# Performance work log

Measured on AMD Instinct MI355X. Metric: run time of the kernel, lower is better.

Reference implementation:

```python
import jax, jax.numpy as jnp
import numpy as np

B, S, D, H, FF = 4, 2048, 1024, 16, 4096
HD = D // H


def setup_inputs() -> dict:
    key = jax.random.key(0)
    ks = jax.random.split(key, 12)
    s = 1.0 / np.sqrt(D)
    sf = 1.0 / np.sqrt(FF)
    return {
        "x": jax.random.normal(ks[0], (B, S, D), dtype=jnp.float32),
        "lengths": jax.random.randint(ks[1], (B,), 1, S + 1, dtype=jnp.int32),
        "qW": jax.random.uniform(ks[2], (D, D), jnp.float32, -s, s),
        "qb": jnp.zeros((D,), jnp.float32),
        "kW": jax.random.uniform(ks[3], (D, D), jnp.float32, -s, s),
        "kb": jnp.zeros((D,), jnp.float32),
        "vW": jax.random.uniform(ks[4], (D, D), jnp.float32, -s, s),
        "vb": jnp.zeros((D,), jnp.float32),
        "oW": jax.random.uniform(ks[5], (D, D), jnp.float32, -s, s),
        "ob": jnp.zeros((D,), jnp.float32),
        "w1": jax.random.uniform(ks[6], (D, FF), jnp.float32, -s, s),
        "b1": jnp.zeros((FF,), jnp.float32),
        "w2": jax.random.uniform(ks[7], (FF, D), jnp.float32, -sf, sf),
        "b2": jnp.zeros((D,), jnp.float32),
    }


def _heads(t):
    # [B,S,D] -> [B,H,S,HD]
    return t.reshape(B, S, H, HD).transpose(0, 2, 1, 3)


def reference(x, lengths, qW, qb, kW, kb, vW, vb, oW, ob, w1, b1, w2, b2):
    q = _heads(x @ qW + qb)
    k = _heads(x @ kW + kb)
    v = _heads(x @ vW + vb)
    scale = 1.0 / np.sqrt(HD)
    logits = jnp.einsum("bhqd,bhkd->bhqk", q, k) * scale  # [B,H,S,S]
    # key-position mask: pos >= length -> -inf
    mask = jnp.arange(S)[None, None, None, :] >= lengths[:, None, None, None]
    logits = jnp.where(mask, -jnp.inf, logits)
    a = jax.nn.softmax(logits, axis=-1)
    ctx = jnp.einsum("bhqk,bhkd->bhqd", a, v)
    ctx = ctx.transpose(0, 2, 1, 3).reshape(B, S, D)
    attn_out = ctx @ oW + ob
    h = jax.nn.relu(attn_out @ w1 + b1)
    return h @ w2 + b2
```

## Files before the change

kernel.cpp:

```cpp
#include <hip/hip_runtime.h>


typedef short bf16x8 __attribute__((ext_vector_type(8)));
typedef float f32x4 __attribute__((ext_vector_type(4)));

__device__ __forceinline__ unsigned short f2bf(float f) {
  unsigned int u = __builtin_bit_cast(unsigned int, f);
  u += 0x7fffu + ((u >> 16) & 1u);
  return (unsigned short)(u >> 16);
}

__device__ __forceinline__ void gload16(const unsigned short* g, unsigned short* l) {
  __builtin_amdgcn_global_load_lds(
      (const __attribute__((address_space(1))) unsigned int*)(g),
      (__attribute__((address_space(3))) unsigned int*)(l),
      16, 0, 0);
}

__global__ __launch_bounds__(256) void cast_f32_bf16(
    const float* __restrict__ src, unsigned short* __restrict__ dst, int n4) {
  int i = blockIdx.x * 256 + threadIdx.x;
  if (i < n4) {
    float4 f = ((const float4*)src)[i];
    ushort4 o;
    o.x = f2bf(f.x); o.y = f2bf(f.y); o.z = f2bf(f.z); o.w = f2bf(f.w);
    ((ushort4*)dst)[i] = o;
  }
}

__global__ __launch_bounds__(256) void prep_weights(
    const float* __restrict__ qW, const float* __restrict__ kW,
    const float* __restrict__ vW, const float* __restrict__ oW,
    const float* __restrict__ w1, const float* __restrict__ w2,
    unsigned short* __restrict__ qWt, unsigned short* __restrict__ kWt,
    unsigned short* __restrict__ vWt, unsigned short* __restrict__ oWt,
    unsigned short* __restrict__ w1t, unsigned short* __restrict__ w2t) {
  const int t = blockIdx.x;
  const float* W; unsigned short* Wt; int N, K, nt, kt;
  if (t < 2048) {
    const int w = t >> 9, r = t & 511;
    nt = r & 15; kt = r >> 4; N = 1024; K = 1024;
    W  = w == 0 ? qW : w == 1 ? kW : w == 2 ? vW : oW;
    Wt = w == 0 ? qWt : w == 1 ? kWt : w == 2 ? vWt : oWt;
  } else if (t < 4096) {
    const int r = t - 2048;
    nt = r & 63; kt = r >> 6; N = 4096; K = 1024; W = w1; Wt = w1t;
  } else {
    const int r = t - 4096;
    nt = r & 15; kt = r >> 4; N = 1024; K = 4096; W = w2; Wt = w2t;
  }
  const int wave = threadIdx.x >> 6, lane = threadIdx.x & 63;
  const int n = nt * 64 + lane;
  const int k0 = kt * 32 + wave * 8;
  union { int4 v; unsigned short u[8]; } s;
#pragma unroll
  for (int j = 0; j < 8; ++j) s.u[j] = f2bf(W[(size_t)(k0 + j) * N + n]);
  *(int4*)(Wt + (size_t)n * K + k0) = s.v;
}

__device__ __forceinline__ void gemm256_8ph(
    const unsigned short* __restrict__ A, const unsigned short* __restrict__ Bt,
    unsigned short* __restrict__ As, unsigned short* __restrict__ Bs,
    const int m0, const int n0, const int K, f32x4 (&acc)[8][4]) {
  const int tid = (int)threadIdx.x;
  const int w = tid >> 6, l = tid & 63;
  const int quad = l >> 4, l16 = l & 15;
  const int wm = (w >> 2) * 128, wn = (w & 3) * 64;

  const int srow = w * 8 + (l >> 3);
  const int schunk = ((l & 7) ^ (l >> 3)) * 8;
  const unsigned short* gA = A + (size_t)(m0 + srow) * K + schunk;
  const unsigned short* gB = Bt + (size_t)(n0 + srow) * K + schunk;
  const int ldsW = w * 512;

  const int xr = l16 & 7;
  const int c0 = ((0 + quad) ^ xr) * 8;
  const int c1 = ((4 + quad) ^ xr) * 8;

  bf16x8 af[4][2], bf0[2][2], bf1[2][2];

  auto STA = [&](int buf, int a, int t) {
    gload16(gA + (size_t)(a * 64) * K + t * 64,
            As + buf * 16384 + a * 4096 + ldsW);
  };
  auto STB = [&](int buf, int a, int t) {
    gload16(gB + (size_t)(a * 64) * K + t * 64,
            Bs + buf * 16384 + a * 4096 + ldsW);
  };
  auto LDA = [&](int buf, int mh) {
    const unsigned short* p = As + buf * 16384 + (wm + mh * 64 + l16) * 64;
#pragma unroll
    for (int mi = 0; mi < 4; ++mi) {
      af[mi][0] = *(const bf16x8*)(p + mi * 16 * 64 + c0);
      af[mi][1] = *(const bf16x8*)(p + mi * 16 * 64 + c1);
    }
  };
  auto LDB = [&](int buf, int nh, bf16x8 (&bf)[2][2]) {
    const unsigned short* p = Bs + buf * 16384 + (wn + nh * 32 + l16) * 64;
#pragma unroll
    for (int ni = 0; ni < 2; ++ni) {
      bf[ni][0] = *(const bf16x8*)(p + ni * 16 * 64 + c0);
      bf[ni][1] = *(const bf16x8*)(p + ni * 16 * 64 + c1);
    }
  };
  auto MM = [&](int mh, int nh, bf16x8 (&bf)[2][2]) {
    __builtin_amdgcn_s_setprio(1);
#pragma unroll
    for (int mi = 0; mi < 4; ++mi)
#pragma unroll
      for (int ni = 0; ni < 2; ++ni) {
        f32x4& a = acc[mh * 4 + mi][nh * 2 + ni];
        a = __builtin_amdgcn_mfma_f32_16x16x32_bf16(af[mi][0], bf[ni][0], a, 0, 0, 0);
        a = __builtin_amdgcn_mfma_f32_16x16x32_bf16(af[mi][1], bf[ni][1], a, 0, 0, 0);
      }
    __builtin_amdgcn_s_setprio(0);
  };

  const int NK = K >> 6;
  STB(0, 0, 0); STB(0, 1, 0); STB(0, 2, 0); STB(0, 3, 0);
  STA(0, 0, 0); STA(0, 2, 0); STA(0, 1, 0); STA(0, 3, 0);
  asm volatile("s_waitcnt vmcnt(2)" ::: "memory");
  __builtin_amdgcn_s_barrier();

#pragma unroll 1
  for (int t = 0; t < NK; ++t) {
    const int c = t & 1, nb = c ^ 1;
    const bool st = (t + 1 < NK);
    LDA(c, 0); LDB(c, 0, bf0);
    if (st) { STB(nb, 0, t + 1); STB(nb, 1, t + 1); }
    __builtin_amdgcn_s_barrier();
    asm volatile("s_waitcnt lgkmcnt(0)" ::: "memory");
    __builtin_amdgcn_sched_barrier(0);
    MM(0, 0, bf0);
    __builtin_amdgcn_s_barrier();
    LDB(c, 1, bf1);
    if (st) { STB(nb, 2, t + 1); STB(nb, 3, t + 1); }
    __builtin_amdgcn_s_barrier();
    asm volatile("s_waitcnt lgkmcnt(0)" ::: "memory");
    __builtin_amdgcn_sched_barrier(0);
    MM(0, 1, bf1);
    if (st) asm volatile("s_waitcnt vmcnt(4)" ::: "memory");
    else    asm volatile("s_waitcnt vmcnt(0)" ::: "memory");
    __builtin_amdgcn_s_barrier();
    LDA(c, 1);
    if (st) { STA(nb, 0, t + 1); STA(nb, 2, t + 1); }
    __builtin_amdgcn_s_barrier();
    asm volatile("s_waitcnt lgkmcnt(0)" ::: "memory");
    __builtin_amdgcn_sched_barrier(0);
    MM(1, 1, bf1);
    __builtin_amdgcn_s_barrier();
    if (st) { STA(nb, 1, t + 1); STA(nb, 3, t + 1); }
    __builtin_amdgcn_s_barrier();
    MM(1, 0, bf0);
    if (st) asm volatile("s_waitcnt vmcnt(2)" ::: "memory");
    __builtin_amdgcn_s_barrier();
  }
}

template <int EPI>
__global__ __launch_bounds__(512, 1) void gemm256_bt(
    const unsigned short* __restrict__ A, const unsigned short* __restrict__ Bt,
    const float* __restrict__ bias, void* __restrict__ C, int N, int K) {
  __shared__ unsigned short As[2 * 16384];
  __shared__ unsigned short Bs[2 * 16384];
  const int tn = N >> 8;
  const int cpx = (int)gridDim.x >> 3;
  const int sw = ((int)blockIdx.x & 7) * cpx + ((int)blockIdx.x >> 3);
  const int nt = sw % tn, mt = sw / tn;
  const int m0 = mt * 256, n0 = nt * 256;

  f32x4 acc[8][4] = {};
  gemm256_8ph(A, Bt, As, Bs, m0, n0, K, acc);

  const int tid = (int)threadIdx.x;
  const int w = tid >> 6, l = tid & 63;
  const int quad = l >> 4, l16 = l & 15;
  const int wm = (w >> 2) * 128, wn = (w & 3) * 64;
#pragma unroll
  for (int ni = 0; ni < 4; ++ni) {
    const int col = n0 + wn + ni * 16 + l16;
    const float bv = bias[col];
#pragma unroll
    for (int mi = 0; mi < 8; ++mi) {
      const int row = m0 + wm + mi * 16 + quad * 4;
#pragma unroll
      for (int r = 0; r < 4; ++r) {
        float v = acc[mi][ni][r] + bv;
        if (EPI == 2) v = v > 0.f ? v : 0.f;
        if (EPI == 0)
          ((float*)C)[(size_t)(row + r) * N + col] = v;
        else
          ((unsigned short*)C)[(size_t)(row + r) * N + col] = f2bf(v);
      }
    }
  }
}

#define QSCALE 0.180336884f

__global__ __launch_bounds__(512, 1) void gemm256_qkv(
    const unsigned short* __restrict__ A, const unsigned short* __restrict__ Bt,
    const float* __restrict__ qb, const float* __restrict__ kb,
    const float* __restrict__ vb, unsigned short* __restrict__ Qo,
    unsigned short* __restrict__ Ko, unsigned short* __restrict__ Vto, int K) {
  __shared__ unsigned short As[2 * 16384];
  __shared__ unsigned short Bs[2 * 16384];
  const int tn = 12;
  const int cpx = (int)gridDim.x >> 3;
  const int sw = ((int)blockIdx.x & 7) * cpx + ((int)blockIdx.x >> 3);
  const int nt = sw % tn, mt = sw / tn;
  const int m0 = mt * 256, n0 = nt * 256;

  f32x4 acc[8][4] = {};
  gemm256_8ph(A, Bt, As, Bs, m0, n0, K, acc);

  const int tid = (int)threadIdx.x;
  const int w = tid >> 6, l = tid & 63;
  const int quad = l >> 4, l16 = l & 15;
  const int wm = (w >> 2) * 128, wn = (w & 3) * 64;

  const int seg = n0 >> 10;
  const float* bias = seg == 0 ? qb : (seg == 1 ? kb : vb);
#pragma unroll
  for (int ni = 0; ni < 4; ++ni) {
    const int col = (n0 + wn + ni * 16 + l16) & 1023;
    const float bv = bias[col];
#pragma unroll
    for (int mi = 0; mi < 8; ++mi) {
      const int row = m0 + wm + mi * 16 + quad * 4;
      if (seg == 2) {
        const int b = row >> 11, s = row & 2047;
        const int hh = col >> 6, dh = col & 63;
        union { ushort4 v; unsigned short u[4]; } pk;
#pragma unroll
        for (int r = 0; r < 4; ++r) pk.u[r] = f2bf(acc[mi][ni][r] + bv);
        *(ushort4*)(Vto + ((size_t)((b * 16 + hh) * 64 + dh)) * 2048 + s) = pk.v;
      } else if (seg == 0) {
#pragma unroll
        for (int r = 0; r < 4; ++r)
          Qo[(size_t)(row + r) * 1024 + col] = f2bf((acc[mi][ni][r] + bv) * QSCALE);
      } else {
#pragma unroll
        for (int r = 0; r < 4; ++r)
          Ko[(size_t)(row + r) * 1024 + col] = f2bf(acc[mi][ni][r] + bv);
      }
    }
  }
}

__device__ __forceinline__ void gemm128_core(
    const unsigned short* __restrict__ A, const unsigned short* __restrict__ Bt,
    unsigned short* __restrict__ As, unsigned short* __restrict__ Bs,
    const int m0, const int n0, const int K, f32x4 (&acc)[4][4]) {
  const int tid = (int)threadIdx.x;
  const int w = tid >> 6, l = tid & 63;
  const int quad = l >> 4, l16 = l & 15;
  const int wm = (w >> 1) * 64, wn = (w & 1) * 64;

  const int lr = l >> 2, lc = l & 3;
  const int swz = (lc ^ ((l >> 3) & 3)) * 8;
  const unsigned short* gA[2]; const unsigned short* gB[2];
  unsigned short* dA[2]; unsigned short* dB[2];
#pragma unroll
  for (int j = 0; j < 2; ++j) {
    const int rr = (w * 2 + j) * 16 + lr;
    gA[j] = A + (size_t)(m0 + rr) * K + swz;
    gB[j] = Bt + (size_t)(n0 + rr) * K + swz;
    dA[j] = As + (w * 2 + j) * 512;
    dB[j] = Bs + (w * 2 + j) * 512;
  }

  const int cread = (quad ^ ((l16 >> 1) & 3)) * 8;
  const int rA = (wm + l16) * 32;
  const int rB = (wn + l16) * 32;

  auto STAGE = [&](int db, int t) {
#pragma unroll
    for (int j = 0; j < 2; ++j) {
      gload16(gA[j] + t * 32, dA[j] + db * 4096);
      gload16(gB[j] + t * 32, dB[j] + db * 4096);
    }
  };
  auto COMPUTE = [&](int db) {
    bf16x8 af[4], bf[4];
    const unsigned short* pa = As + db * 4096 + rA + cread;
    const unsigned short* pb = Bs + db * 4096 + rB + cread;
#pragma unroll
    for (int ni = 0; ni < 4; ++ni) bf[ni] = *(const bf16x8*)(pb + ni * 16 * 32);
#pragma unroll
    for (int mi = 0; mi < 4; ++mi) af[mi] = *(const bf16x8*)(pa + mi * 16 * 32);
    __builtin_amdgcn_s_setprio(1);
#pragma unroll
    for (int mi = 0; mi < 4; ++mi)
#pragma unroll
      for (int ni = 0; ni < 4; ++ni)
        acc[mi][ni] = __builtin_amdgcn_mfma_f32_16x16x32_bf16(
            af[mi], bf[ni], acc[mi][ni], 0, 0, 0);
    __builtin_amdgcn_s_setprio(0);
  };

  const int NK = K >> 5;
  STAGE(0, 0); STAGE(1, 1); STAGE(2, 2);
#pragma unroll 1
  for (int t = 0; t < NK - 3; ++t) {
    asm volatile("s_waitcnt vmcnt(8)" ::: "memory");
    __builtin_amdgcn_s_barrier();
    STAGE((t + 3) & 3, t + 3);
    COMPUTE(t & 3);
  }
  asm volatile("s_waitcnt vmcnt(8)" ::: "memory");
  __builtin_amdgcn_s_barrier();
  COMPUTE((NK - 3) & 3);
  asm volatile("s_waitcnt vmcnt(4)" ::: "memory");
  __builtin_amdgcn_s_barrier();
  COMPUTE((NK - 2) & 3);
  asm volatile("s_waitcnt vmcnt(0)" ::: "memory");
  __builtin_amdgcn_s_barrier();
  COMPUTE((NK - 1) & 3);
}

template <int EPI>
__global__ __launch_bounds__(256, 2) void gemm128_bt(
    const unsigned short* __restrict__ A, const unsigned short* __restrict__ Bt,
    const float* __restrict__ bias, void* __restrict__ C, int N, int K) {
  __shared__ unsigned short As[4 * 4096];
  __shared__ unsigned short Bs[4 * 4096];
  const int NT = N >> 7, band = NT >> 3;
  const int xcd = blockIdx.x & 7, local = blockIdx.x >> 3;
  const int nt = xcd * band + local % band;
  const int mt = local / band;
  const int m0 = mt * 128, n0 = nt * 128;

  f32x4 acc[4][4] = {};
  gemm128_core(A, Bt, As, Bs, m0, n0, K, acc);

  const int tid = (int)threadIdx.x;
  const int w = tid >> 6, l = tid & 63;
  const int quad = l >> 4, l16 = l & 15;
  const int wm = (w >> 1) * 64, wn = (w & 1) * 64;
#pragma unroll
  for (int ni = 0; ni < 4; ++ni) {
    const int col = n0 + wn + ni * 16 + l16;
    const float bv = bias[col];
#pragma unroll
    for (int mi = 0; mi < 4; ++mi) {
      const int row = m0 + wm + mi * 16 + quad * 4;
#pragma unroll
      for (int r = 0; r < 4; ++r) {
        float v = acc[mi][ni][r] + bv;
        if (EPI == 2) v = v > 0.f ? v : 0.f;
        if (EPI == 0)
          ((float*)C)[(size_t)(row + r) * N + col] = v;
        else
          ((unsigned short*)C)[(size_t)(row + r) * N + col] = f2bf(v);
      }
    }
  }
}

__global__ __launch_bounds__(256, 4) void attn_fused(
    const unsigned short* __restrict__ Q, const unsigned short* __restrict__ K,
    const unsigned short* __restrict__ Vt, const int* __restrict__ lengths,
    unsigned short* __restrict__ ctx) {
  constexpr int S = 2048, D = 1024;
  __shared__ unsigned short Ks[64 * 72];
  __shared__ unsigned short Vs[64 * 72];
  __shared__ unsigned short Ps[4 * 32 * 72];

  const int tid = threadIdx.x;
  const int wave = tid >> 6, lane = tid & 63;
  const int quad = lane >> 4, l16 = lane & 15;
  const int bid = blockIdx.x;
  const int qt = bid & 15;
  const int h = (bid >> 4) & 15;
  const int b = bid >> 8;
  const int q0 = qt * 128;
  const int len = lengths[b];
  const int ktEnd = (len + 63) >> 6;
  const float NEGINF = -__builtin_inff();

  const size_t xbase = (size_t)b * S * D + (size_t)h * 64;
  const size_t vtb = (size_t)(b * 16 + h) * 64;

  bf16x8 qf0[2], qf1[2];
#pragma unroll
  for (int mb = 0; mb < 2; ++mb) {
    const unsigned short* qrow =
        Q + xbase + (size_t)(q0 + wave * 32 + mb * 16 + l16) * D;
    qf0[mb] = *(const bf16x8*)(qrow + quad * 8);
    qf1[mb] = *(const bf16x8*)(qrow + 32 + quad * 8);
  }

  const int sr1 = tid >> 3, sc1 = (tid & 7) * 8;
  const int sr2 = (256 + tid) >> 3, sc2 = (tid & 7) * 8;
  const unsigned short* kg1 = K + xbase + (size_t)sr1 * D + sc1;
  const unsigned short* kg2 = K + xbase + (size_t)sr2 * D + sc2;
  const unsigned short* vg1 = Vt + (vtb + sr1) * S + sc1;
  const unsigned short* vg2 = Vt + (vtb + sr2) * S + sc2;

  f32x4 oacc[2][4] = {};
  float rs[2][4] = {};

  unsigned short* pw = Ps + wave * (32 * 72);

  int4 kr1, kr2, vr1, vr2;
  {
    kr1 = *(const int4*)(kg1);
    kr2 = *(const int4*)(kg2);
    vr1 = *(const int4*)(vg1);
    vr2 = *(const int4*)(vg2);
  }

  for (int kt = 0; kt < ktEnd; ++kt) {
    const int k0 = kt * 64;
    __syncthreads();
    *(int4*)(Ks + sr1 * 72 + sc1) = kr1;
    *(int4*)(Ks + sr2 * 72 + sc2) = kr2;
    *(int4*)(Vs + sr1 * 72 + sc1) = vr1;
    *(int4*)(Vs + sr2 * 72 + sc2) = vr2;
    __syncthreads();

    if (kt + 1 < ktEnd) {
      const int kn = (kt + 1) * 64;
      kr1 = *(const int4*)(kg1 + (size_t)kn * D);
      kr2 = *(const int4*)(kg2 + (size_t)kn * D);
      vr1 = *(const int4*)(vg1 + kn);
      vr2 = *(const int4*)(vg2 + kn);
    }

    f32x4 sf[2][4];
#pragma unroll
    for (int cb = 0; cb < 4; ++cb) {
      const bf16x8 kf0 = *(const bf16x8*)(Ks + (cb * 16 + l16) * 72 + quad * 8);
      const bf16x8 kf1 = *(const bf16x8*)(Ks + (cb * 16 + l16) * 72 + 32 + quad * 8);
#pragma unroll
      for (int mb = 0; mb < 2; ++mb) {
        f32x4 c = {0.f, 0.f, 0.f, 0.f};
        c = __builtin_amdgcn_mfma_f32_16x16x32_bf16(qf0[mb], kf0, c, 0, 0, 0);
        c = __builtin_amdgcn_mfma_f32_16x16x32_bf16(qf1[mb], kf1, c, 0, 0, 0);
        sf[mb][cb] = c;
      }
    }

    if (k0 + 64 > len) {
#pragma unroll
      for (int cb = 0; cb < 4; ++cb) {
        const bool msk = (k0 + cb * 16 + l16) >= len;
#pragma unroll
        for (int mb = 0; mb < 2; ++mb)
#pragma unroll
          for (int r = 0; r < 4; ++r) sf[mb][cb][r] = msk ? NEGINF : sf[mb][cb][r];
      }
    }

#pragma unroll
    for (int mb = 0; mb < 2; ++mb)
#pragma unroll
      for (int cb = 0; cb < 4; ++cb)
#pragma unroll
        for (int r = 0; r < 4; ++r) {
          const float p = __builtin_amdgcn_exp2f(sf[mb][cb][r]);
          sf[mb][cb][r] = p;
          rs[mb][r] += p;
        }

#pragma unroll
    for (int mb = 0; mb < 2; ++mb)
#pragma unroll
      for (int cb = 0; cb < 4; ++cb)
#pragma unroll
        for (int r = 0; r < 4; ++r)
          pw[(mb * 16 + quad * 4 + r) * 72 + cb * 16 + l16] = f2bf(sf[mb][cb][r]);

    bf16x8 pa0[2], pa1[2];
#pragma unroll
    for (int mb = 0; mb < 2; ++mb) {
      pa0[mb] = *(const bf16x8*)(pw + (mb * 16 + l16) * 72 + quad * 8);
      pa1[mb] = *(const bf16x8*)(pw + (mb * 16 + l16) * 72 + 32 + quad * 8);
    }
#pragma unroll
    for (int cb = 0; cb < 4; ++cb) {
      const bf16x8 vb0 = *(const bf16x8*)(Vs + (cb * 16 + l16) * 72 + quad * 8);
      const bf16x8 vb1 = *(const bf16x8*)(Vs + (cb * 16 + l16) * 72 + 32 + quad * 8);
#pragma unroll
      for (int mb = 0; mb < 2; ++mb) {
        oacc[mb][cb] = __builtin_amdgcn_mfma_f32_16x16x32_bf16(pa0[mb], vb0, oacc[mb][cb], 0, 0, 0);
        oacc[mb][cb] = __builtin_amdgcn_mfma_f32_16x16x32_bf16(pa1[mb], vb1, oacc[mb][cb], 0, 0, 0);
      }
    }
  }

#pragma unroll
  for (int off = 8; off > 0; off >>= 1)
#pragma unroll
    for (int mb = 0; mb < 2; ++mb)
#pragma unroll
      for (int r = 0; r < 4; ++r) rs[mb][r] += __shfl_xor(rs[mb][r], off, 16);

#pragma unroll
  for (int mb = 0; mb < 2; ++mb) {
    float inv[4];
#pragma unroll
    for (int r = 0; r < 4; ++r) inv[r] = 1.0f / rs[mb][r];
#pragma unroll
    for (int cb = 0; cb < 4; ++cb)
#pragma unroll
      for (int r = 0; r < 4; ++r) {
        const int row = q0 + wave * 32 + mb * 16 + quad * 4 + r;
        ctx[xbase + (size_t)row * D + cb * 16 + l16] = f2bf(oacc[mb][cb][r] * inv[r]);
      }
  }
}

extern "C" void kernel_launch(void* const* d_in, const int* in_sizes, int n_in,
                              void* d_out, int out_size, void* d_ws,
                              size_t ws_size, hipStream_t stream) {
  const float* x  = (const float*)d_in[0];
  const int* lengths = (const int*)d_in[1];
  const float* qW = (const float*)d_in[2];
  const float* qb = (const float*)d_in[3];
  const float* kW = (const float*)d_in[4];
  const float* kb = (const float*)d_in[5];
  const float* vW = (const float*)d_in[6];
  const float* vb = (const float*)d_in[7];
  const float* oW = (const float*)d_in[8];
  const float* ob = (const float*)d_in[9];
  const float* w1 = (const float*)d_in[10];
  const float* b1 = (const float*)d_in[11];
  const float* w2 = (const float*)d_in[12];
  const float* b2 = (const float*)d_in[13];
  float* out = (float*)d_out;

  const int Bx = 4, S = 2048, D = 1024, FF = 4096;
  const int M = Bx * S;

  unsigned short* p = (unsigned short*)d_ws;
  unsigned short* xb  = p; p += (size_t)M * D;
  unsigned short* qWt = p; p += (size_t)D * D;
  unsigned short* kWt = p; p += (size_t)D * D;
  unsigned short* vWt = p; p += (size_t)D * D;
  unsigned short* oWt = p; p += (size_t)D * D;
  unsigned short* w1t = p; p += (size_t)D * FF;
  unsigned short* w2t = p; p += (size_t)FF * D;
  unsigned short* Qb  = p; p += (size_t)M * D;
  unsigned short* Kb  = p; p += (size_t)M * D;
  unsigned short* Vtb = p; p += (size_t)M * D;
  unsigned short* Cb  = p; p += (size_t)M * D;
  unsigned short* Ab  = p; p += (size_t)M * D;
  unsigned short* Hb  = p; p += (size_t)M * FF;

  {
    int n4 = (int)((size_t)M * D / 4);
    cast_f32_bf16<<<dim3((n4 + 255) / 256), dim3(256), 0, stream>>>(x, xb, n4);
  }
  prep_weights<<<dim3(6144), dim3(256), 0, stream>>>(
      qW, kW, vW, oW, w1, w2, qWt, kWt, vWt, oWt, w1t, w2t);

  gemm256_qkv<<<dim3(384), dim3(512), 0, stream>>>(
      xb, qWt, qb, kb, vb, Qb, Kb, Vtb, D);

  attn_fused<<<dim3(Bx * 16 * (S / 128)), dim3(256), 0, stream>>>(
      Qb, Kb, Vtb, lengths, Cb);

  gemm128_bt<1><<<dim3(512), dim3(256), 0, stream>>>(Cb, oWt, ob, Ab, D, D);
  gemm256_bt<2><<<dim3(512), dim3(512), 0, stream>>>(Ab, w1t, b1, Hb, FF, D);
  gemm128_bt<0><<<dim3(512), dim3(256), 0, stream>>>(Hb, w2t, b2, out, D, FF);
}
```

Before: 490.6 us.

## Shrink GEMM pipeline to three LDS stages and move QKV projection to 128-tile kernel

Cuts the 128x128 GEMM core's LDS ring from four stages to three, with prefetch depth two, so three blocks fit per CU (launch bounds raised to 3). The fused QKV projection now uses this 128-tile kernel with 1536 blocks instead of the 256x256 8-phase kernel with 384 blocks. The aim is better occupancy and load balance across CUs. In exchange, the shallower prefetch gives less latency hiding and the smaller tiles reuse data less.

Result: faster. 477.3 us (-2.7%).

```diff
diff --git a/kernel.cpp b/kernel.cpp
--- a/kernel.cpp
+++ b/kernel.cpp
@@ -196,58 +196,6 @@
   }
 }
 
-#define QSCALE 0.180336884f
-
-__global__ __launch_bounds__(512, 1) void gemm256_qkv(
-    const unsigned short* __restrict__ A, const unsigned short* __restrict__ Bt,
-    const float* __restrict__ qb, const float* __restrict__ kb,
-    const float* __restrict__ vb, unsigned short* __restrict__ Qo,
-    unsigned short* __restrict__ Ko, unsigned short* __restrict__ Vto, int K) {
-  __shared__ unsigned short As[2 * 16384];
-  __shared__ unsigned short Bs[2 * 16384];
-  const int tn = 12;
-  const int cpx = (int)gridDim.x >> 3;
-  const int sw = ((int)blockIdx.x & 7) * cpx + ((int)blockIdx.x >> 3);
-  const int nt = sw % tn, mt = sw / tn;
-  const int m0 = mt * 256, n0 = nt * 256;
-
-  f32x4 acc[8][4] = {};
-  gemm256_8ph(A, Bt, As, Bs, m0, n0, K, acc);
-
-  const int tid = (int)threadIdx.x;
-  const int w = tid >> 6, l = tid & 63;
-  const int quad = l >> 4, l16 = l & 15;
-  const int wm = (w >> 2) * 128, wn = (w & 3) * 64;
-
-  const int seg = n0 >> 10;
-  const float* bias = seg == 0 ? qb : (seg == 1 ? kb : vb);
-#pragma unroll
-  for (int ni = 0; ni < 4; ++ni) {
-    const int col = (n0 + wn + ni * 16 + l16) & 1023;
-    const float bv = bias[col];
-#pragma unroll
-    for (int mi = 0; mi < 8; ++mi) {
-      const int row = m0 + wm + mi * 16 + quad * 4;
-      if (seg == 2) {
-        const int b = row >> 11, s = row & 2047;
-        const int hh = col >> 6, dh = col & 63;
-        union { ushort4 v; unsigned short u[4]; } pk;
-#pragma unroll
-        for (int r = 0; r < 4; ++r) pk.u[r] = f2bf(acc[mi][ni][r] + bv);
-        *(ushort4*)(Vto + ((size_t)((b * 16 + hh) * 64 + dh)) * 2048 + s) = pk.v;
-      } else if (seg == 0) {
-#pragma unroll
-        for (int r = 0; r < 4; ++r)
-          Qo[(size_t)(row + r) * 1024 + col] = f2bf((acc[mi][ni][r] + bv) * QSCALE);
-      } else {
-#pragma unroll
-        for (int r = 0; r < 4; ++r)
-          Ko[(size_t)(row + r) * 1024 + col] = f2bf(acc[mi][ni][r] + bv);
-      }
-    }
-  }
-}
-
 __device__ __forceinline__ void gemm128_core(
     const unsigned short* __restrict__ A, const unsigned short* __restrict__ Bt,
     unsigned short* __restrict__ As, unsigned short* __restrict__ Bs,
@@ -300,31 +248,32 @@
   };
 
   const int NK = K >> 5;
-  STAGE(0, 0); STAGE(1, 1); STAGE(2, 2);
+  STAGE(0, 0); STAGE(1, 1);
+  int cc = 0, cs = 2;
 #pragma unroll 1
-  for (int t = 0; t < NK - 3; ++t) {
-    asm volatile("s_waitcnt vmcnt(8)" ::: "memory");
-    __builtin_amdgcn_s_barrier();
-    STAGE((t + 3) & 3, t + 3);
-    COMPUTE(t & 3);
-  }
-  asm volatile("s_waitcnt vmcnt(8)" ::: "memory");
-  __builtin_amdgcn_s_barrier();
-  COMPUTE((NK - 3) & 3);
+  for (int t = 0; t < NK - 2; ++t) {
+    asm volatile("s_waitcnt vmcnt(4)" ::: "memory");
+    __builtin_amdgcn_s_barrier();
+    STAGE(cs, t + 2);
+    COMPUTE(cc);
+    cc = cc == 2 ? 0 : cc + 1;
+    cs = cs == 2 ? 0 : cs + 1;
+  }
   asm volatile("s_waitcnt vmcnt(4)" ::: "memory");
   __builtin_amdgcn_s_barrier();
-  COMPUTE((NK - 2) & 3);
+  COMPUTE(cc);
+  cc = cc == 2 ? 0 : cc + 1;
   asm volatile("s_waitcnt vmcnt(0)" ::: "memory");
   __builtin_amdgcn_s_barrier();
-  COMPUTE((NK - 1) & 3);
+  COMPUTE(cc);
 }
 
 template <int EPI>
-__global__ __launch_bounds__(256, 2) void gemm128_bt(
+__global__ __launch_bounds__(256, 3) void gemm128_bt(
     const unsigned short* __restrict__ A, const unsigned short* __restrict__ Bt,
     const float* __restrict__ bias, void* __restrict__ C, int N, int K) {
-  __shared__ unsigned short As[4 * 4096];
-  __shared__ unsigned short Bs[4 * 4096];
+  __shared__ unsigned short As[3 * 4096];
+  __shared__ unsigned short Bs[3 * 4096];
   const int NT = N >> 7, band = NT >> 3;
   const int xcd = blockIdx.x & 7, local = blockIdx.x >> 3;
   const int nt = xcd * band + local % band;
@@ -353,6 +302,58 @@
           ((float*)C)[(size_t)(row + r) * N + col] = v;
         else
           ((unsigned short*)C)[(size_t)(row + r) * N + col] = f2bf(v);
+      }
+    }
+  }
+}
+
+#define QSCALE 0.180336884f
+
+__global__ __launch_bounds__(256, 3) void gemm128_qkv(
+    const unsigned short* __restrict__ A, const unsigned short* __restrict__ Bt,
+    const float* __restrict__ qb, const float* __restrict__ kb,
+    const float* __restrict__ vb, unsigned short* __restrict__ Qo,
+    unsigned short* __restrict__ Ko, unsigned short* __restrict__ Vto, int K) {
+  __shared__ unsigned short As[3 * 4096];
+  __shared__ unsigned short Bs[3 * 4096];
+  const int NT = 24, band = 3;
+  const int xcd = blockIdx.x & 7, local = blockIdx.x >> 3;
+  const int nt = xcd * band + local % band;
+  const int mt = local / band;
+  const int m0 = mt * 128, n0 = nt * 128;
+
+  f32x4 acc[4][4] = {};
+  gemm128_core(A, Bt, As, Bs, m0, n0, K, acc);
+
+  const int tid = (int)threadIdx.x;
+  const int w = tid >> 6, l = tid & 63;
+  const int quad = l >> 4, l16 = l & 15;
+  const int wm = (w >> 1) * 64, wn = (w & 1) * 64;
+
+  const int seg = n0 >> 10;
+  const float* bias = seg == 0 ? qb : (seg == 1 ? kb : vb);
+#pragma unroll
+  for (int ni = 0; ni < 4; ++ni) {
+    const int col = (n0 + wn + ni * 16 + l16) & 1023;
+    const float bv = bias[col];
+#pragma unroll
+    for (int mi = 0; mi < 4; ++mi) {
+      const int row = m0 + wm + mi * 16 + quad * 4;
+      if (seg == 2) {
+        const int b = row >> 11, s = row & 2047;
+        const int hh = col >> 6, dh = col & 63;
+        union { ushort4 v; unsigned short u[4]; } pk;
+#pragma unroll
+        for (int r = 0; r < 4; ++r) pk.u[r] = f2bf(acc[mi][ni][r] + bv);
+        *(ushort4*)(Vto + ((size_t)((b * 16 + hh) * 64 + dh)) * 2048 + s) = pk.v;
+      } else if (seg == 0) {
+#pragma unroll
+        for (int r = 0; r < 4; ++r)
+          Qo[(size_t)(row + r) * 1024 + col] = f2bf((acc[mi][ni][r] + bv) * QSCALE);
+      } else {
+#pragma unroll
+        for (int r = 0; r < 4; ++r)
+          Ko[(size_t)(row + r) * 1024 + col] = f2bf(acc[mi][ni][r] + bv);
       }
     }
   }
@@ -556,7 +557,7 @@
   prep_weights<<<dim3(6144), dim3(256), 0, stream>>>(
       qW, kW, vW, oW, w1, w2, qWt, kWt, vWt, oWt, w1t, w2t);
 
-  gemm256_qkv<<<dim3(384), dim3(512), 0, stream>>>(
+  gemm128_qkv<<<dim3(1536), dim3(256), 0, stream>>>(
       xb, qWt, qb, kb, vb, Qb, Kb, Vtb, D);
 
   attn_fused<<<dim3(Bx * 16 * (S / 128)), dim3(256), 0, stream>>>(
```
